# Optimization experiments

Measured on AMD Instinct MI355X. Metric: run time of the kernel, lower is better.

Reference implementation:

```python
import jax, jax.numpy as jnp
import numpy as np
from jax import lax

RATE = 2          # self.rate
KS = 3            # kernel_size for matching patches
FUSE_K = 3        # fuse_k
SCALE = 10.0      # softmax_scale
EPS = 1e-4        # NaN guard in l2 norm


def extract_patches(x, size=3, step=1):
    """ZeroPad2d(1) then unfold -> (B, L, C, size, size) with L = Ho*Wo."""
    B, C, H, W = x.shape
    p = lax.conv_general_dilated_patches(
        x, (size, size), (step, step), padding=((1, 1), (1, 1)))
    Ho, Wo = p.shape[2], p.shape[3]
    # feature dim ordering of patches is (C, kh, kw)
    p = p.reshape(B, C, size, size, Ho, Wo)
    return p.transpose(0, 4, 5, 1, 2, 3).reshape(B, Ho * Wo, C, size, size)


def fuse_conv(s):
    """Conv with identity eye(k) kernel, pad 1 (diagonal propagation)."""
    w = jnp.eye(FUSE_K, dtype=s.dtype).reshape(1, 1, FUSE_K, FUSE_K)
    return lax.conv_general_dilated(s, w, (1, 1), ((1, 1), (1, 1)))


def contextual_attention(foreground, background, mask):
    B, C, H, W = foreground.shape
    # raw patches used as deconv filters: (B, L, C, 2*rate, 2*rate)
    raw_w = extract_patches(background, size=2 * RATE, step=RATE)
    # nearest downsample by rate (F.interpolate nearest, scale 1/rate == stride slice)
    fg = foreground[:, :, ::RATE, ::RATE]
    bg = background[:, :, ::RATE, ::RATE]
    fh, fw = fg.shape[2], fg.shape[3]
    bh, bw = bg.shape[2], bg.shape[3]
    # matching patches: (B, L, C, 3, 3), L = bh*bw
    w = extract_patches(bg, KS, 1)
    # mask patches -> per-patch validity (code uses batch 0 of the mask only)
    m = mask[:, :, ::RATE, ::RATE]
    mp = extract_patches(m, KS, 1)[0]            # (L, 1, 3, 3)
    mm = jnp.mean(mp, axis=(1, 2, 3))            # (L,)
    eq = (mm == 0.0).astype(foreground.dtype)[None, :, None, None]  # (1, L, 1, 1)
    # cosine-normalized filters
    norm = jnp.sqrt(jnp.sum(w * w, axis=(2, 3, 4), keepdims=True))
    wn = w / jnp.maximum(norm, EPS)
    # per-batch dynamic conv: scores (B, L, fh, fw)
    def score(f, wi):
        return lax.conv_general_dilated(f[None], wi, (1, 1), ((1, 1), (1, 1)))[0]
    s = jax.vmap(score)(fg, wn)
    # fuse: two identity-kernel convs with raw reshapes (faithful to torch .view,
    # including the discarded second permute in the original code)
    s = s.reshape(B, 1, fh * fw, bh * bw)
    s = fuse_conv(s)
    s = s.reshape(B, fh, fw, bh, bw).transpose(0, 2, 1, 4, 3)
    s = s.reshape(B, 1, fh * fw, bh * bw)
    s = fuse_conv(s)
    s = s.reshape(B, bh * bw, fh, fw)  # raw row-major reinterpret, as torch .view does
    # masked scaled softmax over background-patch dim
    s = s * eq
    s = jax.nn.softmax(s * SCALE, axis=1) * eq
    # per-batch deconv with raw patches as filters (conv_transpose2d stride=rate, pad=1)
    def deconv(si, rwi):
        # torch conv_transpose2d(W:(L,C,4,4)) == dilated conv with flipped, swapped kernel
        wt = jnp.flip(rwi, axis=(-2, -1)).transpose(1, 0, 2, 3)  # (C, L, 4, 4)
        pad = 2 * RATE - 1 - 1  # k - 1 - padding = 2
        return lax.conv_general_dilated(
            si[None], wt, (1, 1), ((pad, pad), (pad, pad)),
            lhs_dilation=(RATE, RATE))[0]
    y = jax.vmap(deconv)(s, raw_w) / 4.0  # (B, C, H, W)
    return y


def setup_inputs() -> dict:
    key = jax.random.key(0)
    k1, k2, k3 = jax.random.split(key, 3)
    B, C, H, W = 8, 128, 64, 64
    foreground = jax.random.normal(k1, (B, C, H, W), jnp.float32)
    background = jax.random.normal(k2, (B, C, H, W), jnp.float32)
    mask = (jax.random.uniform(k3, (1, 1, H, W)) < 0.25).astype(jnp.float32)
    return {"foreground": foreground, "background": background, "mask": mask}


def reference(foreground, background, mask):
    return contextual_attention(foreground, background, mask)
```

## Files before the change

### kernel.cpp

```cpp
#include <hip/hip_runtime.h>

typedef _Float16 half8 __attribute__((ext_vector_type(8)));
typedef float f32x4 __attribute__((ext_vector_type(4)));
typedef unsigned short us8 __attribute__((ext_vector_type(8)));
typedef unsigned short ush;
typedef unsigned int uint32;

#define IMGB 295936u
#define WROW 8704u

#define OFF_FGH  0ull
#define OFF_BGH  2367488ull
#define OFF_BGL  4734976ull
#define OFF_BGT  7102464ull
#define OFF_RN   15491072ull
#define OFF_LIST 15589376ull
#define OFF_NACT 15593472ull
#define OFF_S0   15597568ull
#define OFF_S2   49152000ull
#define OFF_WGT2 82706432ull

static __device__ __forceinline__ ush f2h(float f) {
    union { _Float16 h; ush u; } c; c.h = (_Float16)f; return c.u;
}
static __device__ __forceinline__ float h2f(ush u) {
    union { _Float16 h; ush u; } c; c.u = u; return (float)c.h;
}
__device__ __forceinline__ int untr(int v) { return ((v & 31) << 5) | (v >> 5); }

__global__ void k_prep2(const float* __restrict__ fg, const float* __restrict__ bg,
                        ush* __restrict__ fgh, ush* __restrict__ bgh,
                        ush* __restrict__ bgl, ush* __restrict__ BGt) {
    int y = blockIdx.x, b = blockIdx.y, t = threadIdx.x;
    __shared__ float lds[64 * 129];
    __shared__ float fls[32 * 129];
    int xx = t & 63;
    for (int c0 = 0; c0 < 128; c0 += 4) {
        int c = c0 + (t >> 6);
        lds[xx * 129 + c] = bg[((b * 128 + c) * 64 + y) * 64 + xx];
    }
    __syncthreads();
    uint32* dst = (uint32*)(BGt + (size_t)(b * 64 + y) * 8192);
    for (int j = t; j < 4096; j += 256) {
        int x = j >> 6, cp = (j & 63) * 2;
        uint32 h0 = f2h(lds[x * 129 + cp]);
        uint32 h1 = f2h(lds[x * 129 + cp + 1]);
        dst[j] = h0 | (h1 << 16);
    }
    if ((y & 1) != 0) return;
    int yd = y >> 1;
    {
        int xq = t & 31, cg = t >> 5;
        for (int c0 = 0; c0 < 128; c0 += 8) {
            int c = c0 + cg;
            fls[xq * 129 + c] = fg[((b * 128 + c) * 64 + y) * 64 + 2 * xq];
        }
    }
    __syncthreads();
    unsigned base = ((b * 34 + yd + 1) * 34 + 1) * 128;
    for (int k = t; k < 2048; k += 256) {
        int x = k >> 6, cp = (k & 63) * 2;
        float vb0 = lds[(2 * x) * 129 + cp], vb1 = lds[(2 * x) * 129 + cp + 1];
        float vf0 = fls[x * 129 + cp],       vf1 = fls[x * 129 + cp + 1];
        _Float16 bh0 = (_Float16)vb0, bh1 = (_Float16)vb1;
        float br0 = vb0 - (float)bh0, br1 = vb1 - (float)bh1;
        uint32 f01 = (uint32)f2h(vf0) | ((uint32)f2h(vf1) << 16);
        union { _Float16 h; ush u; } x0, x1;
        x0.h = bh0; x1.h = bh1;
        uint32 b01 = (uint32)x0.u | ((uint32)x1.u << 16);
        uint32 l01 = (uint32)f2h(br0) | ((uint32)f2h(br1) << 16);
        ((uint32*)(fgh + base))[k] = f01;
        ((uint32*)(bgh + base))[k] = b01;
        ((uint32*)(bgl + base))[k] = l01;
    }
    unsigned cb0 = ((unsigned)(b * 34 + yd + 1) * 34) * 64;
    if (t < 64) {
        ((uint32*)fgh)[cb0 + t] = 0; ((uint32*)bgh)[cb0 + t] = 0; ((uint32*)bgl)[cb0 + t] = 0;
    } else if (t < 128) {
        unsigned cb1 = cb0 + 33 * 64 + (t - 64);
        ((uint32*)fgh)[cb1] = 0; ((uint32*)bgh)[cb1] = 0; ((uint32*)bgl)[cb1] = 0;
    }
    if (yd == 0 || yd == 31) {
        int prow = (yd == 0) ? 0 : 33;
        unsigned rb = (unsigned)(b * 34 + prow) * 2176;
        for (int k = t; k < 2176; k += 256) {
            ((uint32*)fgh)[rb + k] = 0; ((uint32*)bgh)[rb + k] = 0; ((uint32*)bgl)[rb + k] = 0;
        }
    }
}

__global__ void k_ssnq(const ush* __restrict__ bgh, const ush* __restrict__ bgl,
                       const float* __restrict__ mask, float* __restrict__ rnorm,
                       int* __restrict__ L, int* __restrict__ nact) {
    int bx = blockIdx.x, b = blockIdx.y, t = threadIdx.x;
    __shared__ float ssh[10][32];
    __shared__ int ps[256];
    if (bx == 4) {
        if (b != 0) return;
        int fl[4], s = 0;
#pragma unroll
        for (int j = 0; j < 4; ++j) {
            int l = t * 4 + j;
            int hm = l >> 5, wm = l & 31;
            int any = 0;
            for (int di = -1; di <= 1; ++di)
                for (int dj = -1; dj <= 1; ++dj) {
                    int yy = hm + di, xxx = wm + dj;
                    if (yy >= 0 && yy < 32 && xxx >= 0 && xxx < 32)
                        any |= (mask[(2 * yy) * 64 + 2 * xxx] != 0.0f);
                }
            fl[j] = !any; s += fl[j];
        }
        ps[t] = s;
        __syncthreads();
        for (int off = 1; off < 256; off <<= 1) {
            int v = (t >= off) ? ps[t - off] : 0;
            __syncthreads();
            ps[t] += v;
            __syncthreads();
        }
        int base = ps[t] - s;
#pragma unroll
        for (int j = 0; j < 4; ++j)
            if (fl[j]) L[base++] = t * 4 + j;
        if (t == 255) nact[0] = ps[255];
        return;
    }
    int r0 = bx * 8;
    for (int idx = t; idx < 320; idx += 256) {
        int row = idx >> 5, xx = idx & 31;
        int gy = r0 - 1 + row;
        float s = 0.f;
        if (gy >= 0 && gy < 32) {
            size_t base = ((size_t)(b * 34 + gy + 1) * 34 + xx + 1) * 128;
            for (int c = 0; c < 128; c += 8) {
                us8 vh = *(const us8*)(bgh + base + c);
                us8 vl = *(const us8*)(bgl + base + c);
#pragma unroll
                for (int j = 0; j < 8; ++j) {
                    float v = h2f(vh[j]) + h2f(vl[j]);
                    s += v * v;
                }
            }
        }
        ssh[row][xx] = s;
    }
    __syncthreads();
    int pr = t >> 5, pc = t & 31;
    float n2 = 0.f;
#pragma unroll
    for (int di = -1; di <= 1; ++di)
#pragma unroll
        for (int dj = -1; dj <= 1; ++dj) {
            int xx = pc + dj;
            if (xx >= 0 && xx < 32) n2 += ssh[pr + 1 + di][xx];
        }
    rnorm[b * 1024 + (r0 + pr) * 32 + pc] = 1.0f / fmaxf(sqrtf(n2), 1e-4f);
}

__global__ __launch_bounds__(256, 2)
void k_smfma(const ush* __restrict__ fgh, const ush* __restrict__ bgh,
             const ush* __restrict__ bgl, const float* __restrict__ rnorm,
             float* __restrict__ s0) {
    int qt = blockIdx.x, pt = blockIdx.y, b = blockIdx.z;
    int t = threadIdx.x, wid = t >> 6, lane = t & 63;
    int wp = wid >> 1, wq = wid & 1;
    __shared__ ulong2 smem_raw[4992];
    char* smem = (char*)smem_raw;

    const char* base0 = (const char*)bgh + (size_t)b * IMGB + (unsigned)(pt * 4) * WROW;
    const char* base1 = (const char*)bgl + (size_t)b * IMGB + (unsigned)(pt * 4) * WROW;
    const char* base2 = (const char*)fgh + (size_t)b * IMGB + (unsigned)(qt * 4) * WROW;

    f32x4 acc[4][4];
#pragma unroll
    for (int i = 0; i < 4; ++i)
#pragma unroll
        for (int j = 0; j < 4; ++j) acc[i][j] = (f32x4){0.f, 0.f, 0.f, 0.f};

    int r15 = lane & 15, hi2 = lane >> 4;
    for (int ch = 0; ch < 2; ++ch) {
        __syncthreads();
        {
            int pixl = (lane >> 3);
            int sl = lane & 7;
            for (int idx = wid; idx < 78; idx += 4) {
                int a = idx / 26;
                int chunk = idx - a * 26;
                int pix = chunk * 8 + pixl;
                int g = sl ^ (pix & 7);
                const char* sb = (a == 0) ? base0 : (a == 1) ? base1 : base2;
                const char* gp = sb + ((unsigned)pix << 8) + ((unsigned)ch << 7)
                               + ((unsigned)g << 4);
                char* lp = smem + (unsigned)(a * 26624 + chunk * 1024);
                __builtin_amdgcn_global_load_lds(
                    (const __attribute__((address_space(1))) void*)gp,
                    (__attribute__((address_space(3))) void*)lp, 16, 0, 0);
            }
        }
        __syncthreads();

        for (int o = 0; o < 9; ++o) {
            int dy = o / 3, dx = o - 3 * (o / 3);
            int pixB[4], pixA[4];
#pragma unroll
            for (int i = 0; i < 4; ++i) {
                pixB[i] = (wp * 2 + (i >> 1) + dy) * 34 + (i & 1) * 16 + r15 + dx;
                pixA[i] = (wq * 2 + (i >> 1) + dy) * 34 + (i & 1) * 16 + r15 + dx;
            }
#pragma unroll
            for (int cc = 0; cc < 2; ++cc) {
                int g = cc * 4 + hi2;
                half8 bh[4], bl[4], af[4];
#pragma unroll
                for (int i = 0; i < 4; ++i) {
                    unsigned offB = ((unsigned)pixB[i] << 7) + ((unsigned)(g ^ (pixB[i] & 7)) << 4);
                    bh[i] = *(const half8*)(smem + offB);
                    bl[i] = *(const half8*)(smem + 26624 + offB);
                    unsigned offA = ((unsigned)pixA[i] << 7) + ((unsigned)(g ^ (pixA[i] & 7)) << 4);
                    af[i] = *(const half8*)(smem + 53248 + offA);
                }
#pragma unroll
                for (int i = 0; i < 4; ++i)
#pragma unroll
                    for (int j = 0; j < 4; ++j) {
                        acc[i][j] = __builtin_amdgcn_mfma_f32_16x16x32_f16(bh[i], af[j], acc[i][j], 0, 0, 0);
                        acc[i][j] = __builtin_amdgcn_mfma_f32_16x16x32_f16(bl[i], af[j], acc[i][j], 0, 0, 0);
                    }
            }
        }
    }
    int col = lane & 15, rgrp = (lane >> 4) << 2;
#pragma unroll
    for (int i = 0; i < 4; ++i) {
        int Pb = pt * 128 + wp * 64 + i * 16 + rgrp;
        float rn0 = rnorm[b * 1024 + Pb + 0];
        float rn1 = rnorm[b * 1024 + Pb + 1];
        float rn2 = rnorm[b * 1024 + Pb + 2];
        float rn3 = rnorm[b * 1024 + Pb + 3];
#pragma unroll
        for (int j = 0; j < 4; ++j) {
            int Q = qt * 128 + wq * 64 + j * 16 + col;
            float* dst = s0 + ((size_t)(b * 1024 + Pb) << 10) + Q;
            dst[0]    = acc[i][j][0] * rn0;
            dst[1024] = acc[i][j][1] * rn1;
            dst[2048] = acc[i][j][2] * rn2;
            dst[3072] = acc[i][j][3] * rn3;
        }
    }
}

__global__ void k_fuse(const float* __restrict__ s0, float* __restrict__ s2t,
                       const int* __restrict__ L, const int* __restrict__ nactp) {
    int nact = *nactp;
    int b = blockIdx.z;
    int u = blockIdx.x * 256 + threadIdx.x;
    int T = untr(u);
    const float* S = s0 + (size_t)b * 1048576;
    for (int ai = blockIdx.y; ai < nact; ai += 32) {
        int R = L[ai];
        float acc = 0.f;
#pragma unroll
        for (int k = -1; k <= 1; ++k) {
            int Rk = R + k, Tk = T + k;
            if ((unsigned)Rk < 1024u && (unsigned)Tk < 1024u) {
                int Pr = untr(Rk), Qc = untr(Tk);
#pragma unroll
                for (int j = -1; j <= 1; ++j) {
                    int r = Pr + j, cI = Qc + j;
                    if ((unsigned)r < 1024u && (unsigned)cI < 1024u)
                        acc += S[(size_t)r * 1024 + cI];
                }
            }
        }
        s2t[(size_t)b * 1048576 + (size_t)R * 1024 + u] = acc;
    }
}

__global__ void k_ct(const ush* __restrict__ BGt, const int* __restrict__ L,
                     const int* __restrict__ nactp, ush* __restrict__ CT) {
    int nact = *nactp;
    int KPAD = (nact + 31) & ~31;
    int ab = blockIdx.x, b = blockIdx.y, t = threadIdx.x;
    int a = ab >> 2, bb = ab & 3;
    for (int ai0 = 0; ai0 < KPAD; ai0 += 256) {
        int ai = ai0 + t;
        if (ai >= KPAD) break;
        int ok = 0;
        const ush* srow = nullptr;
        if (ai < nact) {
            int R = L[ai];
            int hb = R >> 5, wb = R & 31;
            int row = 2 * hb - 1 + a, col = 2 * wb - 1 + bb;
            if (row >= 0 && row < 64 && col >= 0 && col < 64) {
                ok = 1;
                srow = BGt + ((size_t)((b * 64 + row) * 64 + col) << 7);
            }
        }
        ush* dst = CT + ((size_t)(b * 16 + ab) << 15) + ai;
#pragma unroll 4
        for (int c = 0; c < 128; ++c)
            dst[(size_t)c << 8] = ok ? srow[c] : (ush)0;
    }
}

__global__ __launch_bounds__(256)
void k_softw(const float* __restrict__ s2t, const int* __restrict__ L,
             const int* __restrict__ nactp, ush* __restrict__ W2) {
    int uc = blockIdx.x, b = blockIdx.y, t = threadIdx.x;
    int nact = *nactp;
    int u0 = uc * 32;
    __shared__ float sm[32][8], sd[32][8];
    __shared__ float Msh[32], RDsh[32];
    __shared__ ush wt[32][136];
    int part = t >> 5, ul = t & 31;
    {
        const float* S = s2t + (size_t)b * 1048576 + u0 + ul;
        float m = -3e38f, d = 0.f;
        for (int ai = part; ai < nact; ai += 8) {
            float v = S[(size_t)L[ai] << 10];
            if (v > m) { d *= expf(10.f * (m - v)); m = v; }
            d += expf(10.f * (v - m));
        }
        sm[ul][part] = m; sd[ul][part] = d;
    }
    __syncthreads();
    if (t < 32) {
        float mm = -3e38f, dd = 0.f;
#pragma unroll
        for (int p = 0; p < 8; ++p) {
            float m2 = sm[t][p], d2 = sd[t][p];
            if (m2 > mm) { dd *= expf(10.f * (mm - m2)); mm = m2; dd += d2; }
            else dd += d2 * expf(10.f * (m2 - mm));
        }
        int cnt0 = 1024 - nact;
        if (cnt0 > 0) {
            if (mm < 0.f) { dd *= expf(10.f * mm); mm = 0.f; }
            dd += (float)cnt0 * expf(-10.f * mm);
        }
        Msh[t] = mm; RDsh[t] = 1.f / dd;
    }
    __syncthreads();
    for (int kp = 0; kp < 16; ++kp) {
        int k = kp * 8 + part;
        float w = 0.f;
        if (k < nact) {
            float v = s2t[((size_t)(b * 1024 + L[k]) << 10) + u0 + ul];
            w = expf(10.f * (v - Msh[ul])) * RDsh[ul];
        }
        wt[ul][k] = f2h(w);
    }
    __syncthreads();
    {
        int ur = t >> 3, kb = t & 7;
        int uu = u0 + ur;
        int p1 = (uu & 31) + 1, q1 = (uu >> 5) + 1;
        ush* dstr = W2 + (((size_t)(b * 35 + p1) * 35 + q1) << 7) + kb * 16;
        *(half8*)dstr       = *(const half8*)&wt[ur][kb * 16];
        *(half8*)(dstr + 8) = *(const half8*)&wt[ur][kb * 16 + 8];
    }
    for (int r = uc; r < 1225; r += 32) {
        int p1 = r / 35, q1 = r - p1 * 35;
        if (p1 < 1 || p1 > 32 || q1 < 1 || q1 > 32) {
            uint32* row = (uint32*)(W2 + (((size_t)(b * 35 + p1) * 35 + q1) << 7));
            if (t < 64) row[t] = 0;
        }
    }
}

__global__ __launch_bounds__(256, 4)
void k_dgemm(const ush* __restrict__ CT, const ush* __restrict__ W2,
             const int* __restrict__ nactp, float* __restrict__ y) {
    int nact = *nactp;
    int KPAD = (nact + 31) & ~31;
    int pt2 = blockIdx.x;
    int par = blockIdx.y, b = blockIdx.z;
    int a_lo = par >> 1, b_lo = par & 1;
    int P0 = 1 - a_lo, Q0 = 1 - b_lo;
    int p_lo = P0 + pt2;
    int wid = threadIdx.x >> 6, lane = threadIdx.x & 63;
    int r15 = lane & 15, kg = (lane >> 4) << 3;

    f32x4 acc[2][2];
#pragma unroll
    for (int i = 0; i < 2; ++i)
#pragma unroll
        for (int j = 0; j < 2; ++j) acc[i][j] = (f32x4){0.f, 0.f, 0.f, 0.f};

    for (int k0 = 0; k0 < KPAD; k0 += 32) {
#pragma unroll
        for (int pp = 0; pp < 2; ++pp)
#pragma unroll
            for (int qq = 0; qq < 2; ++qq) {
                int ab = (a_lo + 2 * pp) * 4 + (b_lo + 2 * qq);
                const ush* Ab = CT + ((size_t)(b * 16 + ab) << 15)
                              + ((unsigned)(wid * 32) << 8) + k0 + kg;
                int p1 = p_lo - pp + 1;
                int q1b = Q0 - qq + 1;
                const ush* Bb = W2 + (((size_t)(b * 35 + p1) * 35 + q1b) << 7) + k0 + kg;
                half8 A[2], B[2];
                A[0] = *(const half8*)(Ab + ((unsigned)r15 << 8));
                A[1] = *(const half8*)(Ab + ((unsigned)(16 + r15) << 8));
                B[0] = *(const half8*)(Bb + ((unsigned)r15 << 7));
                B[1] = *(const half8*)(Bb + ((unsigned)(16 + r15) << 7));
#pragma unroll
                for (int i = 0; i < 2; ++i)
#pragma unroll
                    for (int j = 0; j < 2; ++j)
                        acc[i][j] = __builtin_amdgcn_mfma_f32_16x16x32_f16(A[i], B[j], acc[i][j], 0, 0, 0);
            }
    }
    int col = r15, rgrp = (lane >> 4) << 2;
    int oy = 2 * p_lo + a_lo - 1;
#pragma unroll
    for (int i = 0; i < 2; ++i) {
        int c = wid * 32 + i * 16 + rgrp;
#pragma unroll
        for (int j = 0; j < 2; ++j) {
            int q_lo = Q0 + j * 16 + col;
            int ox = 2 * q_lo + b_lo - 1;
            float* Y = y + ((size_t)((b * 128 + c) * 64 + oy) << 6) + ox;
            Y[0]         = acc[i][j][0] * 0.25f;
            Y[4096]      = acc[i][j][1] * 0.25f;
            Y[2 * 4096]  = acc[i][j][2] * 0.25f;
            Y[3 * 4096]  = acc[i][j][3] * 0.25f;
        }
    }
}

extern "C" void kernel_launch(void* const* d_in, const int* in_sizes, int n_in,
                              void* d_out, int out_size, void* d_ws, size_t ws_size,
                              hipStream_t stream) {
    (void)in_sizes; (void)n_in; (void)out_size; (void)ws_size;
    const float* fg   = (const float*)d_in[0];
    const float* bg   = (const float*)d_in[1];
    const float* mask = (const float*)d_in[2];
    float* y = (float*)d_out;
    char* ws = (char*)d_ws;

    ush*   fgh   = (ush*)(ws + OFF_FGH);
    ush*   bgh   = (ush*)(ws + OFF_BGH);
    ush*   bgl   = (ush*)(ws + OFF_BGL);
    ush*   BGt   = (ush*)(ws + OFF_BGT);
    float* rnorm = (float*)(ws + OFF_RN);
    int*   Lst   = (int*)(ws + OFF_LIST);
    int*   nact  = (int*)(ws + OFF_NACT);
    float* s0    = (float*)(ws + OFF_S0);
    ush*   CT    = (ush*)(ws + OFF_S0);
    float* s2t   = (float*)(ws + OFF_S2);
    ush*   W2    = (ush*)(ws + OFF_WGT2);

    k_prep2<<<dim3(64, 8), 256, 0, stream>>>(fg, bg, fgh, bgh, bgl, BGt);
    k_ssnq<<<dim3(5, 8), 256, 0, stream>>>(bgh, bgl, mask, rnorm, Lst, nact);
    k_smfma<<<dim3(8, 8, 8), 256, 0, stream>>>(fgh, bgh, bgl, rnorm, s0);
    k_fuse<<<dim3(4, 32, 8), 256, 0, stream>>>(s0, s2t, Lst, nact);
    k_ct<<<dim3(16, 8), 256, 0, stream>>>(BGt, Lst, nact, CT);
    k_softw<<<dim3(32, 8), 256, 0, stream>>>(s2t, Lst, nact, W2);
    k_dgemm<<<dim3(32, 4, 8), 256, 0, stream>>>(CT, W2, nact, y);
}
```

Measured before the change: 125.2 us.

## Split score GEMM over channel halves, read fg from planar global layout, merge ct/softw

The score kernel now splits the two 64-channel halves across separate blocks, doubling the grid, and writes two partial score buffers that the fuse kernel sums. Foreground fp16 data is stored in a new plane-per-channel-group layout and read straight from global memory instead of staged in LDS. This shrinks shared memory and lets three blocks fit per CU. The CT-transpose and softmax-weight kernels are merged into one launch. The cost is an extra 32MB partial buffer that must be written and then read back in the fuse stage.

```diff
diff --git a/kernel.cpp b/kernel.cpp
--- a/kernel.cpp
+++ b/kernel.cpp
@@ -19,6 +19,7 @@
 #define OFF_S0   15597568ull
 #define OFF_S2   49152000ull
 #define OFF_WGT2 82706432ull
+#define OFF_S0B  85215232ull
 
 static __device__ __forceinline__ ush f2h(float f) {
     union { _Float16 h; ush u; } c; c.h = (_Float16)f; return c.u;
@@ -29,7 +30,7 @@
 __device__ __forceinline__ int untr(int v) { return ((v & 31) << 5) | (v >> 5); }
 
 __global__ void k_prep2(const float* __restrict__ fg, const float* __restrict__ bg,
-                        ush* __restrict__ fgh, ush* __restrict__ bgh,
+                        ush* __restrict__ fgh3, ush* __restrict__ bgh,
                         ush* __restrict__ bgl, ush* __restrict__ BGt) {
     int y = blockIdx.x, b = blockIdx.y, t = threadIdx.x;
     __shared__ float lds[64 * 129];
@@ -59,32 +60,43 @@
     __syncthreads();
     unsigned base = ((b * 34 + yd + 1) * 34 + 1) * 128;
     for (int k = t; k < 2048; k += 256) {
-        int x = k >> 6, cp = (k & 63) * 2;
-        float vb0 = lds[(2 * x) * 129 + cp], vb1 = lds[(2 * x) * 129 + cp + 1];
-        float vf0 = fls[x * 129 + cp],       vf1 = fls[x * 129 + cp + 1];
+        int x = k >> 6, c = (k & 63) * 2;
+        float vb0 = lds[(2 * x) * 129 + c], vb1 = lds[(2 * x) * 129 + c + 1];
+        float vf0 = fls[x * 129 + c],       vf1 = fls[x * 129 + c + 1];
         _Float16 bh0 = (_Float16)vb0, bh1 = (_Float16)vb1;
         float br0 = vb0 - (float)bh0, br1 = vb1 - (float)bh1;
-        uint32 f01 = (uint32)f2h(vf0) | ((uint32)f2h(vf1) << 16);
         union { _Float16 h; ush u; } x0, x1;
         x0.h = bh0; x1.h = bh1;
         uint32 b01 = (uint32)x0.u | ((uint32)x1.u << 16);
         uint32 l01 = (uint32)f2h(br0) | ((uint32)f2h(br1) << 16);
-        ((uint32*)(fgh + base))[k] = f01;
         ((uint32*)(bgh + base))[k] = b01;
         ((uint32*)(bgl + base))[k] = l01;
+        uint32 f01 = (uint32)f2h(vf0) | ((uint32)f2h(vf1) << 16);
+        int ch = c >> 6, g = (c >> 3) & 7, cl = c & 7;
+        unsigned pix = (unsigned)(yd + 1) * 34 + (x + 1);
+        unsigned ui = (((unsigned)(b * 16 + ch * 8 + g) * 1156 + pix) << 2) + (cl >> 1);
+        ((uint32*)fgh3)[ui] = f01;
     }
     unsigned cb0 = ((unsigned)(b * 34 + yd + 1) * 34) * 64;
     if (t < 64) {
-        ((uint32*)fgh)[cb0 + t] = 0; ((uint32*)bgh)[cb0 + t] = 0; ((uint32*)bgl)[cb0 + t] = 0;
+        ((uint32*)bgh)[cb0 + t] = 0; ((uint32*)bgl)[cb0 + t] = 0;
     } else if (t < 128) {
         unsigned cb1 = cb0 + 33 * 64 + (t - 64);
-        ((uint32*)fgh)[cb1] = 0; ((uint32*)bgh)[cb1] = 0; ((uint32*)bgl)[cb1] = 0;
+        ((uint32*)bgh)[cb1] = 0; ((uint32*)bgl)[cb1] = 0;
+    } else if (t < 256) {
+        int tt = t - 128;
+        unsigned pix = (unsigned)(yd + 1) * 34 + ((tt >> 6) ? 33u : 0u);
+        int pl = tt & 63, plane = pl >> 2, w = pl & 3;
+        ((uint32*)fgh3)[(((unsigned)(b * 16 + plane) * 1156 + pix) << 2) + w] = 0;
     }
     if (yd == 0 || yd == 31) {
         int prow = (yd == 0) ? 0 : 33;
         unsigned rb = (unsigned)(b * 34 + prow) * 2176;
         for (int k = t; k < 2176; k += 256) {
-            ((uint32*)fgh)[rb + k] = 0; ((uint32*)bgh)[rb + k] = 0; ((uint32*)bgl)[rb + k] = 0;
+            ((uint32*)bgh)[rb + k] = 0; ((uint32*)bgl)[rb + k] = 0;
+            int plane = k / 136, rem = k - plane * 136;
+            unsigned pix = (unsigned)prow * 34 + (rem >> 2);
+            ((uint32*)fgh3)[(((unsigned)(b * 16 + plane) * 1156 + pix) << 2) + (rem & 3)] = 0;
         }
     }
 }
@@ -158,19 +170,38 @@
     rnorm[b * 1024 + (r0 + pr) * 32 + pc] = 1.0f / fmaxf(sqrtf(n2), 1e-4f);
 }
 
-__global__ __launch_bounds__(256, 2)
-void k_smfma(const ush* __restrict__ fgh, const ush* __restrict__ bgh,
+__global__ __launch_bounds__(256, 3)
+void k_smfma(const ush* __restrict__ fgh3, const ush* __restrict__ bgh,
              const ush* __restrict__ bgl, const float* __restrict__ rnorm,
-             float* __restrict__ s0) {
-    int qt = blockIdx.x, pt = blockIdx.y, b = blockIdx.z;
+             float* __restrict__ s0a, float* __restrict__ s0b) {
+    int qt = blockIdx.x, pt = blockIdx.y, z = blockIdx.z;
+    int b = z >> 1, ch = z & 1;
     int t = threadIdx.x, wid = t >> 6, lane = t & 63;
     int wp = wid >> 1, wq = wid & 1;
-    __shared__ ulong2 smem_raw[4992];
+    __shared__ ulong2 smem_raw[3328];
     char* smem = (char*)smem_raw;
 
     const char* base0 = (const char*)bgh + (size_t)b * IMGB + (unsigned)(pt * 4) * WROW;
     const char* base1 = (const char*)bgl + (size_t)b * IMGB + (unsigned)(pt * 4) * WROW;
-    const char* base2 = (const char*)fgh + (size_t)b * IMGB + (unsigned)(qt * 4) * WROW;
+
+    {
+        int pixl = (lane >> 3);
+        int sl = lane & 7;
+        for (int idx = wid; idx < 52; idx += 4) {
+            int a = idx / 26;
+            int chunk = idx - a * 26;
+            int pix = chunk * 8 + pixl;
+            int g = sl ^ (pix & 7);
+            const char* sb = a ? base1 : base0;
+            const char* gp = sb + ((unsigned)pix << 8) + ((unsigned)ch << 7)
+                           + ((unsigned)g << 4);
+            char* lp = smem + (unsigned)(a * 26624 + chunk * 1024);
+            __builtin_amdgcn_global_load_lds(
+                (const __attribute__((address_space(1))) void*)gp,
+                (__attribute__((address_space(3))) void*)lp, 16, 0, 0);
+        }
+    }
+    __syncthreads();
 
     f32x4 acc[4][4];
 #pragma unroll
@@ -179,57 +210,37 @@
         for (int j = 0; j < 4; ++j) acc[i][j] = (f32x4){0.f, 0.f, 0.f, 0.f};
 
     int r15 = lane & 15, hi2 = lane >> 4;
-    for (int ch = 0; ch < 2; ++ch) {
-        __syncthreads();
-        {
-            int pixl = (lane >> 3);
-            int sl = lane & 7;
-            for (int idx = wid; idx < 78; idx += 4) {
-                int a = idx / 26;
-                int chunk = idx - a * 26;
-                int pix = chunk * 8 + pixl;
-                int g = sl ^ (pix & 7);
-                const char* sb = (a == 0) ? base0 : (a == 1) ? base1 : base2;
-                const char* gp = sb + ((unsigned)pix << 8) + ((unsigned)ch << 7)
-                               + ((unsigned)g << 4);
-                char* lp = smem + (unsigned)(a * 26624 + chunk * 1024);
-                __builtin_amdgcn_global_load_lds(
-                    (const __attribute__((address_space(1))) void*)gp,
-                    (__attribute__((address_space(3))) void*)lp, 16, 0, 0);
+    const char* Aimg = (const char*)fgh3
+                     + (((size_t)(b * 16 + ch * 8)) * 1156 + (unsigned)(qt * 136)) * 16;
+    for (int o = 0; o < 9; ++o) {
+        int dy = o / 3, dx = o - 3 * (o / 3);
+        int pixB[4], pixA[4];
+#pragma unroll
+        for (int i = 0; i < 4; ++i) {
+            pixB[i] = (wp * 2 + (i >> 1) + dy) * 34 + (i & 1) * 16 + r15 + dx;
+            pixA[i] = (wq * 2 + (i >> 1) + dy) * 34 + (i & 1) * 16 + r15 + dx;
+        }
+#pragma unroll
+        for (int cc = 0; cc < 2; ++cc) {
+            int g = cc * 4 + hi2;
+            half8 bh[4], bl[4], af[4];
+#pragma unroll
+            for (int i = 0; i < 4; ++i) {
+                unsigned offB = ((unsigned)pixB[i] << 7) + ((unsigned)(g ^ (pixB[i] & 7)) << 4);
+                bh[i] = *(const half8*)(smem + offB);
+                bl[i] = *(const half8*)(smem + 26624 + offB);
+                af[i] = *(const half8*)(Aimg + (((size_t)g * 1156 + pixA[i]) << 4));
             }
-        }
-        __syncthreads();
-
-        for (int o = 0; o < 9; ++o) {
-            int dy = o / 3, dx = o - 3 * (o / 3);
-            int pixB[4], pixA[4];
-#pragma unroll
-            for (int i = 0; i < 4; ++i) {
-                pixB[i] = (wp * 2 + (i >> 1) + dy) * 34 + (i & 1) * 16 + r15 + dx;
-                pixA[i] = (wq * 2 + (i >> 1) + dy) * 34 + (i & 1) * 16 + r15 + dx;
-            }
-#pragma unroll
-            for (int cc = 0; cc < 2; ++cc) {
-                int g = cc * 4 + hi2;
-                half8 bh[4], bl[4], af[4];
-#pragma unroll
-                for (int i = 0; i < 4; ++i) {
-                    unsigned offB = ((unsigned)pixB[i] << 7) + ((unsigned)(g ^ (pixB[i] & 7)) << 4);
-                    bh[i] = *(const half8*)(smem + offB);
-                    bl[i] = *(const half8*)(smem + 26624 + offB);
-                    unsigned offA = ((unsigned)pixA[i] << 7) + ((unsigned)(g ^ (pixA[i] & 7)) << 4);
-                    af[i] = *(const half8*)(smem + 53248 + offA);
+#pragma unroll
+            for (int i = 0; i < 4; ++i)
+#pragma unroll
+                for (int j = 0; j < 4; ++j) {
+                    acc[i][j] = __builtin_amdgcn_mfma_f32_16x16x32_f16(bh[i], af[j], acc[i][j], 0, 0, 0);
+                    acc[i][j] = __builtin_amdgcn_mfma_f32_16x16x32_f16(bl[i], af[j], acc[i][j], 0, 0, 0);
                 }
-#pragma unroll
-                for (int i = 0; i < 4; ++i)
-#pragma unroll
-                    for (int j = 0; j < 4; ++j) {
-                        acc[i][j] = __builtin_amdgcn_mfma_f32_16x16x32_f16(bh[i], af[j], acc[i][j], 0, 0, 0);
-                        acc[i][j] = __builtin_amdgcn_mfma_f32_16x16x32_f16(bl[i], af[j], acc[i][j], 0, 0, 0);
-                    }
-            }
-        }
-    }
+        }
+    }
+    float* s0p = ch ? s0b : s0a;
     int col = lane & 15, rgrp = (lane >> 4) << 2;
 #pragma unroll
     for (int i = 0; i < 4; ++i) {
@@ -241,7 +252,7 @@
 #pragma unroll
         for (int j = 0; j < 4; ++j) {
             int Q = qt * 128 + wq * 64 + j * 16 + col;
-            float* dst = s0 + ((size_t)(b * 1024 + Pb) << 10) + Q;
+            float* dst = s0p + ((size_t)(b * 1024 + Pb) << 10) + Q;
             dst[0]    = acc[i][j][0] * rn0;
             dst[1024] = acc[i][j][1] * rn1;
             dst[2048] = acc[i][j][2] * rn2;
@@ -250,13 +261,15 @@
     }
 }
 
-__global__ void k_fuse(const float* __restrict__ s0, float* __restrict__ s2t,
+__global__ void k_fuse(const float* __restrict__ s0a, const float* __restrict__ s0b,
+                       float* __restrict__ s2t,
                        const int* __restrict__ L, const int* __restrict__ nactp) {
     int nact = *nactp;
     int b = blockIdx.z;
     int u = blockIdx.x * 256 + threadIdx.x;
     int T = untr(u);
-    const float* S = s0 + (size_t)b * 1048576;
+    const float* Sa = s0a + (size_t)b * 1048576;
+    const float* Sb = s0b + (size_t)b * 1048576;
     for (int ai = blockIdx.y; ai < nact; ai += 32) {
         int R = L[ai];
         float acc = 0.f;
@@ -268,8 +281,10 @@
 #pragma unroll
                 for (int j = -1; j <= 1; ++j) {
                     int r = Pr + j, cI = Qc + j;
-                    if ((unsigned)r < 1024u && (unsigned)cI < 1024u)
-                        acc += S[(size_t)r * 1024 + cI];
+                    if ((unsigned)r < 1024u && (unsigned)cI < 1024u) {
+                        size_t o = (size_t)r * 1024 + cI;
+                        acc += Sa[o] + Sb[o];
+                    }
                 }
             }
         }
@@ -277,42 +292,41 @@
     }
 }
 
-__global__ void k_ct(const ush* __restrict__ BGt, const int* __restrict__ L,
-                     const int* __restrict__ nactp, ush* __restrict__ CT) {
+__global__ __launch_bounds__(256)
+void k_ctsw(const ush* __restrict__ BGt, const float* __restrict__ s2t,
+            const int* __restrict__ L, const int* __restrict__ nactp,
+            ush* __restrict__ CT, ush* __restrict__ W2) {
+    int bx = blockIdx.x, b = blockIdx.y, t = threadIdx.x;
     int nact = *nactp;
-    int KPAD = (nact + 31) & ~31;
-    int ab = blockIdx.x, b = blockIdx.y, t = threadIdx.x;
-    int a = ab >> 2, bb = ab & 3;
-    for (int ai0 = 0; ai0 < KPAD; ai0 += 256) {
-        int ai = ai0 + t;
-        if (ai >= KPAD) break;
-        int ok = 0;
-        const ush* srow = nullptr;
-        if (ai < nact) {
-            int R = L[ai];
-            int hb = R >> 5, wb = R & 31;
-            int row = 2 * hb - 1 + a, col = 2 * wb - 1 + bb;
-            if (row >= 0 && row < 64 && col >= 0 && col < 64) {
-                ok = 1;
-                srow = BGt + ((size_t)((b * 64 + row) * 64 + col) << 7);
-            }
-        }
-        ush* dst = CT + ((size_t)(b * 16 + ab) << 15) + ai;
-#pragma unroll 4
-        for (int c = 0; c < 128; ++c)
-            dst[(size_t)c << 8] = ok ? srow[c] : (ush)0;
-    }
-}
-
-__global__ __launch_bounds__(256)
-void k_softw(const float* __restrict__ s2t, const int* __restrict__ L,
-             const int* __restrict__ nactp, ush* __restrict__ W2) {
-    int uc = blockIdx.x, b = blockIdx.y, t = threadIdx.x;
-    int nact = *nactp;
-    int u0 = uc * 32;
     __shared__ float sm[32][8], sd[32][8];
     __shared__ float Msh[32], RDsh[32];
     __shared__ ush wt[32][136];
+    if (bx < 16) {
+        int KPAD = (nact + 31) & ~31;
+        int ab = bx, a = ab >> 2, bb = ab & 3;
+        for (int ai0 = 0; ai0 < KPAD; ai0 += 256) {
+            int ai = ai0 + t;
+            if (ai >= KPAD) break;
+            int ok = 0;
+            const ush* srow = nullptr;
+            if (ai < nact) {
+                int R = L[ai];
+                int hb = R >> 5, wb = R & 31;
+                int row = 2 * hb - 1 + a, col = 2 * wb - 1 + bb;
+                if (row >= 0 && row < 64 && col >= 0 && col < 64) {
+                    ok = 1;
+                    srow = BGt + ((size_t)((b * 64 + row) * 64 + col) << 7);
+                }
+            }
+            ush* dst = CT + ((size_t)(b * 16 + ab) << 15) + ai;
+#pragma unroll 4
+            for (int c = 0; c < 128; ++c)
+                dst[(size_t)c << 8] = ok ? srow[c] : (ush)0;
+        }
+        return;
+    }
+    int uc = bx - 16;
+    int u0 = uc * 32;
     int part = t >> 5, ul = t & 31;
     {
         const float* S = s2t + (size_t)b * 1048576 + u0 + ul;
@@ -438,23 +452,23 @@
     float* y = (float*)d_out;
     char* ws = (char*)d_ws;
 
-    ush*   fgh   = (ush*)(ws + OFF_FGH);
+    ush*   fgh3  = (ush*)(ws + OFF_FGH);
     ush*   bgh   = (ush*)(ws + OFF_BGH);
     ush*   bgl   = (ush*)(ws + OFF_BGL);
     ush*   BGt   = (ush*)(ws + OFF_BGT);
     float* rnorm = (float*)(ws + OFF_RN);
     int*   Lst   = (int*)(ws + OFF_LIST);
     int*   nact  = (int*)(ws + OFF_NACT);
-    float* s0    = (float*)(ws + OFF_S0);
+    float* s0a   = (float*)(ws + OFF_S0);
+    float* s0b   = (float*)(ws + OFF_S0B);
     ush*   CT    = (ush*)(ws + OFF_S0);
     float* s2t   = (float*)(ws + OFF_S2);
     ush*   W2    = (ush*)(ws + OFF_WGT2);
 
-    k_prep2<<<dim3(64, 8), 256, 0, stream>>>(fg, bg, fgh, bgh, bgl, BGt);
+    k_prep2<<<dim3(64, 8), 256, 0, stream>>>(fg, bg, fgh3, bgh, bgl, BGt);
     k_ssnq<<<dim3(5, 8), 256, 0, stream>>>(bgh, bgl, mask, rnorm, Lst, nact);
-    k_smfma<<<dim3(8, 8, 8), 256, 0, stream>>>(fgh, bgh, bgl, rnorm, s0);
-    k_fuse<<<dim3(4, 32, 8), 256, 0, stream>>>(s0, s2t, Lst, nact);
-    k_ct<<<dim3(16, 8), 256, 0, stream>>>(BGt, Lst, nact, CT);
-    k_softw<<<dim3(32, 8), 256, 0, stream>>>(s2t, Lst, nact, W2);
+    k_smfma<<<dim3(8, 8, 16), 256, 0, stream>>>(fgh3, bgh, bgl, rnorm, s0a, s0b);
+    k_fuse<<<dim3(4, 32, 8), 256, 0, stream>>>(s0a, s0b, s2t, Lst, nact);
+    k_ctsw<<<dim3(48, 8), 256, 0, stream>>>(BGt, s2t, Lst, nact, CT, W2);
     k_dgemm<<<dim3(32, 4, 8), 256, 0, stream>>>(CT, W2, nact, y);
 }
```

After: 119.9 us. 4.3% less time.
